# Kernel tuning notes

Measured on AMD Instinct MI355X. Metric: run time of the kernel, lower is better.

## Reference

```python
import jax, jax.numpy as jnp
import numpy as np

EPS_NORM = 1e-12  # torch F.normalize clamp_min eps
EPS_LOG = 1e-10


def setup_inputs() -> dict:
    key = jax.random.key(0)
    k1, k2 = jax.random.split(key)
    N, D = 12288, 128
    embeddings = jax.random.uniform(k1, (N, D), dtype=jnp.float32)
    adj = jax.random.uniform(k2, (N, N), dtype=jnp.float32)
    lambda_reg = jnp.float32(1.0)
    return {"embeddings": embeddings, "adj": adj, "lambda_reg": lambda_reg}


def reference(embeddings, adj, lambda_reg):
    # F.normalize(embeddings, dim=1, p=4): x / max(||x||_4, eps)
    norm4 = jnp.power(jnp.sum(jnp.abs(embeddings) ** 4, axis=1, keepdims=True), 0.25)
    e = embeddings / jnp.maximum(norm4, EPS_NORM)          # [N, D]
    log_p = jnp.log(e + EPS_LOG)                           # [N, D]
    p_log_p = jnp.sum(e * log_p, axis=1)                   # [N]
    cross = e @ log_p.T                                    # [N, N]
    kl = p_log_p[:, None] - cross                          # [N, N]
    # F.normalize(adj, p=1, dim=1): row-wise L1 normalization
    adj_n = adj / jnp.maximum(jnp.sum(jnp.abs(adj), axis=1, keepdims=True), EPS_NORM)
    return lambda_reg * jnp.sum(kl * adj_n)
```

## Files before the change

### kernel.cpp

```cpp
#include <hip/hip_runtime.h>
#include <hip/hip_bf16.h>

#define EPSN 1e-12f
#define EPSL 1e-10f
#define KSPLIT 64
#define KS 64

typedef __attribute__((ext_vector_type(8))) short short8;
typedef __attribute__((ext_vector_type(4))) float f32x4;

__device__ __forceinline__ unsigned short f2bf_rne(float f) {
  union { float f; unsigned u; } x; x.f = f;
  unsigned r = x.u + 0x7FFFu + ((x.u >> 16) & 1u);
  return (unsigned short)(r >> 16);
}

__global__ __launch_bounds__(256)
void prep_kernel(const float* __restrict__ emb, float* __restrict__ e,
                 unsigned short* __restrict__ lpB, float* __restrict__ plp,
                 float* __restrict__ S, float* __restrict__ v, int N) {
  int w = threadIdx.x >> 6, l = threadIdx.x & 63;
  int row = blockIdx.x * 4 + w;
  if (row >= N) return;
  const float* x = emb + (size_t)row * 128;
  float2 xv = *(const float2*)(x + 2 * l);
  float s4 = xv.x*xv.x*xv.x*xv.x + xv.y*xv.y*xv.y*xv.y;
  #pragma unroll
  for (int m = 1; m < 64; m <<= 1) s4 += __shfl_xor(s4, m);
  float denom = fmaxf(sqrtf(sqrtf(s4)), EPSN);
  float e0 = xv.x / denom, e1 = xv.y / denom;
  float lp0 = logf(e0 + EPSL), lp1 = logf(e1 + EPSL);
  e[(size_t)row * 128 + 2*l]     = e0;
  e[(size_t)row * 128 + 2*l + 1] = e1;
  int ksr = row >> 5, lhir = (row >> 3) & 3, jr = row & 7;
  int d0 = 2 * l, d1 = 2 * l + 1;
  lpB[((size_t)(ksr*8 + (d0>>4))*64 + (d0&15) + 16*lhir)*8 + jr] = f2bf_rne(lp0);
  lpB[((size_t)(ksr*8 + (d1>>4))*64 + (d1&15) + 16*lhir)*8 + jr] = f2bf_rne(lp1);
  float pl = e0 * lp0 + e1 * lp1;
  #pragma unroll
  for (int m = 1; m < 64; m <<= 1) pl += __shfl_xor(pl, m);
  if (l == 0) { plp[row] = pl; S[row] = 0.f; v[row] = 0.f; }
}

__global__ __launch_bounds__(256, 2)
void gemm_kernel(const float* __restrict__ adj, const float* __restrict__ e,
                 const unsigned short* __restrict__ lpB,
                 float* __restrict__ S, float* __restrict__ v, int N) {
  __shared__ unsigned short bsh[KS * 3 * 128];
  int w = threadIdx.x >> 6, l = threadIdx.x & 63;
  int l16 = l & 15, lhi = l >> 4;
  int wrow0 = blockIdx.x * 128 + w * 32;
  int kr = N / KSPLIT;
  int k0 = blockIdx.y * kr;
  int nsteps = kr / KS;

  {
    const short8* gB = (const short8*)(lpB + (size_t)k0 * 128);
    short8* sB = (short8*)bsh;
    #pragma unroll
    for (int i = 0; i < 12; ++i) {
      int idx = (w * 12 + i) * 64 + l;
      sB[idx] = gB[idx];
    }
  }

  f32x4 acc[2][8];
  #pragma unroll
  for (int i = 0; i < 2; ++i)
    #pragma unroll
    for (int j = 0; j < 8; ++j) acc[i][j] = (f32x4){0.f, 0.f, 0.f, 0.f};
  float sAcc[2] = {0.f, 0.f};

  const float* rp0 = adj + (size_t)(wrow0 + l16) * N + k0 + lhi * 8;
  const float* rp1 = rp0 + (size_t)16 * N;

  float4 ra[2][2][2], rb[2][2][2];

#define LOADA(buf, s)                                                   \
  {                                                                     \
    _Pragma("unroll")                                                   \
    for (int rt_ = 0; rt_ < 2; ++rt_) {                                 \
      const float* bp_ = (rt_ ? rp1 : rp0) + (s) * KS;                  \
      _Pragma("unroll")                                                 \
      for (int ks_ = 0; ks_ < 2; ++ks_) {                               \
        buf[rt_][ks_][0] = *(const float4*)(bp_ + ks_ * 32);            \
        buf[rt_][ks_][1] = *(const float4*)(bp_ + ks_ * 32 + 4);        \
      }                                                                 \
    }                                                                   \
  }

#define STEP(buf, s)                                                    \
  {                                                                     \
    _Pragma("unroll")                                                   \
    for (int ks_ = 0; ks_ < 2; ++ks_) {                                 \
      short8 bb_[8];                                                    \
      _Pragma("unroll")                                                 \
      for (int ct_ = 0; ct_ < 8; ++ct_)                                 \
        bb_[ct_] = *((const short8*)bsh + ((size_t)(((s)*2 + ks_)*8 + ct_))*64 + l); \
      short8 af_[2];                                                    \
      _Pragma("unroll")                                                 \
      for (int rt_ = 0; rt_ < 2; ++rt_) {                               \
        float4 x0_ = buf[rt_][ks_][0], x1_ = buf[rt_][ks_][1];          \
        sAcc[rt_] += ((x0_.x + x0_.y) + (x0_.z + x0_.w)) +              \
                     ((x1_.x + x1_.y) + (x1_.z + x1_.w));               \
        short8 t_;                                                      \
        t_[0] = (short)f2bf_rne(x0_.x); t_[1] = (short)f2bf_rne(x0_.y); \
        t_[2] = (short)f2bf_rne(x0_.z); t_[3] = (short)f2bf_rne(x0_.w); \
        t_[4] = (short)f2bf_rne(x1_.x); t_[5] = (short)f2bf_rne(x1_.y); \
        t_[6] = (short)f2bf_rne(x1_.z); t_[7] = (short)f2bf_rne(x1_.w); \
        af_[rt_] = t_;                                                  \
      }                                                                 \
      _Pragma("unroll")                                                 \
      for (int ct_ = 0; ct_ < 8; ++ct_) {                               \
        acc[0][ct_] = __builtin_amdgcn_mfma_f32_16x16x32_bf16(af_[0], bb_[ct_], acc[0][ct_], 0, 0, 0); \
        acc[1][ct_] = __builtin_amdgcn_mfma_f32_16x16x32_bf16(af_[1], bb_[ct_], acc[1][ct_], 0, 0, 0); \
      }                                                                 \
    }                                                                   \
  }

  LOADA(ra, 0);
  __syncthreads();

  for (int s = 0; s < nsteps; s += 2) {
    if (s + 1 < nsteps) LOADA(rb, s + 1);
    STEP(ra, s);
    if (s + 2 < nsteps) LOADA(ra, s + 2);
    if (s + 1 < nsteps) STEP(rb, s + 1);
  }

  #pragma unroll
  for (int rt = 0; rt < 2; ++rt) {
    float s = sAcc[rt];
    s += __shfl_xor(s, 16);
    s += __shfl_xor(s, 32);
    if (l < 16) atomicAdd(&S[wrow0 + rt * 16 + l], s);
  }

  #pragma unroll
  for (int rt = 0; rt < 2; ++rt) {
    #pragma unroll
    for (int r = 0; r < 4; ++r) {
      int row = wrow0 + rt * 16 + lhi * 4 + r;
      float p = 0.f;
      #pragma unroll
      for (int ct = 0; ct < 8; ++ct)
        p += e[(size_t)row * 128 + ct * 16 + l16] * acc[rt][ct][r];
      p += __shfl_xor(p, 1);
      p += __shfl_xor(p, 2);
      p += __shfl_xor(p, 4);
      p += __shfl_xor(p, 8);
      if (l16 == 0) atomicAdd(&v[row], p);
    }
  }
}

__global__ __launch_bounds__(1024)
void final_kernel(const float* __restrict__ plp, const float* __restrict__ S,
                  const float* __restrict__ v, const float* __restrict__ lam,
                  float* __restrict__ out, int N) {
  __shared__ float red[16];
  float acc = 0.f;
  for (int i = threadIdx.x; i < N; i += 1024) {
    float s = S[i], d = fmaxf(s, EPSN);
    acc += plp[i] * (s / d) - v[i] / d;
  }
  #pragma unroll
  for (int m = 1; m < 64; m <<= 1) acc += __shfl_xor(acc, m);
  int w = threadIdx.x >> 6, l = threadIdx.x & 63;
  if (l == 0) red[w] = acc;
  __syncthreads();
  if (threadIdx.x == 0) {
    float t = 0.f;
    #pragma unroll
    for (int i = 0; i < 16; ++i) t += red[i];
    out[0] = lam[0] * t;
  }
}

extern "C" void kernel_launch(void* const* d_in, const int* in_sizes, int n_in,
                              void* d_out, int out_size, void* d_ws, size_t ws_size,
                              hipStream_t stream) {
  const float* emb = (const float*)d_in[0];
  const float* adj = (const float*)d_in[1];
  const float* lam = (const float*)d_in[2];
  int N = in_sizes[0] / 128;

  char* ws = (char*)d_ws;
  float* e            = (float*)ws;
  unsigned short* lpB = (unsigned short*)(ws + (size_t)N * 512);
  float* plp          = (float*)(ws + (size_t)N * 768);
  float* S            = plp + N;
  float* v            = S + N;

  prep_kernel<<<(N + 3) / 4, 256, 0, stream>>>(emb, e, lpB, plp, S, v, N);
  dim3 grid(N / 128, KSPLIT);
  gemm_kernel<<<grid, 256, 0, stream>>>(adj, e, lpB, S, v, N);
  final_kernel<<<1, 1024, 0, stream>>>(plp, S, v, lam, (float*)d_out, N);
}
```

Measured before the change: 205.6 us.

## Stream B tiles through double-buffered LDS and reduce K-split count

```diff
diff --git a/kernel.cpp b/kernel.cpp
--- a/kernel.cpp
+++ b/kernel.cpp
@@ -3,7 +3,7 @@
 
 #define EPSN 1e-12f
 #define EPSL 1e-10f
-#define KSPLIT 64
+#define KSPLIT 16
 #define KS 64
 
 typedef __attribute__((ext_vector_type(8))) short short8;
@@ -42,27 +42,17 @@
   if (l == 0) { plp[row] = pl; S[row] = 0.f; v[row] = 0.f; }
 }
 
-__global__ __launch_bounds__(256, 2)
+__global__ __launch_bounds__(256, 3)
 void gemm_kernel(const float* __restrict__ adj, const float* __restrict__ e,
                  const unsigned short* __restrict__ lpB,
                  float* __restrict__ S, float* __restrict__ v, int N) {
-  __shared__ unsigned short bsh[KS * 3 * 128];
+  __shared__ unsigned short bsh[2][KS * 128];
   int w = threadIdx.x >> 6, l = threadIdx.x & 63;
   int l16 = l & 15, lhi = l >> 4;
   int wrow0 = blockIdx.x * 128 + w * 32;
   int kr = N / KSPLIT;
   int k0 = blockIdx.y * kr;
-  int nsteps = kr / KS;
-
-  {
-    const short8* gB = (const short8*)(lpB + (size_t)k0 * 128);
-    short8* sB = (short8*)bsh;
-    #pragma unroll
-    for (int i = 0; i < 12; ++i) {
-      int idx = (w * 12 + i) * 64 + l;
-      sB[idx] = gB[idx];
-    }
-  }
+  int nt = kr / KS;
 
   f32x4 acc[2][8];
   #pragma unroll
@@ -74,13 +64,14 @@
   const float* rp0 = adj + (size_t)(wrow0 + l16) * N + k0 + lhi * 8;
   const float* rp1 = rp0 + (size_t)16 * N;
 
-  float4 ra[2][2][2], rb[2][2][2];
-
-#define LOADA(buf, s)                                                   \
+  float4 aset0[2][2][2], aset1[2][2][2];
+  float4 rBs[2][4];
+
+#define LOADA(buf, t)                                                   \
   {                                                                     \
     _Pragma("unroll")                                                   \
     for (int rt_ = 0; rt_ < 2; ++rt_) {                                 \
-      const float* bp_ = (rt_ ? rp1 : rp0) + (s) * KS;                  \
+      const float* bp_ = (rt_ ? rp1 : rp0) + (t) * KS;                  \
       _Pragma("unroll")                                                 \
       for (int ks_ = 0; ks_ < 2; ++ks_) {                               \
         buf[rt_][ks_][0] = *(const float4*)(bp_ + ks_ * 32);            \
@@ -89,18 +80,35 @@
     }                                                                   \
   }
 
-#define STEP(buf, s)                                                    \
+#define LOADB(dst, t)                                                   \
+  {                                                                     \
+    const char* p_ = (const char*)lpB + (((size_t)(k0 + (t) * KS)) << 8) \
+                     + w * 4096 + l * 16;                               \
+    _Pragma("unroll")                                                   \
+    for (int i_ = 0; i_ < 4; ++i_)                                      \
+      dst[i_] = *(const float4*)(p_ + i_ * 1024);                       \
+  }
+
+#define WRITEB(bi, src)                                                 \
+  {                                                                     \
+    char* q_ = (char*)bsh[bi] + w * 4096 + l * 16;                      \
+    _Pragma("unroll")                                                   \
+    for (int i_ = 0; i_ < 4; ++i_)                                      \
+      *(float4*)(q_ + i_ * 1024) = src[i_];                             \
+  }
+
+#define STEP(abuf, bi)                                                  \
   {                                                                     \
     _Pragma("unroll")                                                   \
     for (int ks_ = 0; ks_ < 2; ++ks_) {                                 \
       short8 bb_[8];                                                    \
       _Pragma("unroll")                                                 \
       for (int ct_ = 0; ct_ < 8; ++ct_)                                 \
-        bb_[ct_] = *((const short8*)bsh + ((size_t)(((s)*2 + ks_)*8 + ct_))*64 + l); \
+        bb_[ct_] = *(const short8*)((char*)bsh[bi] + (ks_*8 + ct_)*1024 + l*16); \
       short8 af_[2];                                                    \
       _Pragma("unroll")                                                 \
       for (int rt_ = 0; rt_ < 2; ++rt_) {                               \
-        float4 x0_ = buf[rt_][ks_][0], x1_ = buf[rt_][ks_][1];          \
+        float4 x0_ = abuf[rt_][ks_][0], x1_ = abuf[rt_][ks_][1];        \
         sAcc[rt_] += ((x0_.x + x0_.y) + (x0_.z + x0_.w)) +              \
                      ((x1_.x + x1_.y) + (x1_.z + x1_.w));               \
         short8 t_;                                                      \
@@ -110,22 +118,41 @@
         t_[6] = (short)f2bf_rne(x1_.z); t_[7] = (short)f2bf_rne(x1_.w); \
         af_[rt_] = t_;                                                  \
       }                                                                 \
+      __builtin_amdgcn_s_setprio(1);                                    \
       _Pragma("unroll")                                                 \
       for (int ct_ = 0; ct_ < 8; ++ct_) {                               \
         acc[0][ct_] = __builtin_amdgcn_mfma_f32_16x16x32_bf16(af_[0], bb_[ct_], acc[0][ct_], 0, 0, 0); \
         acc[1][ct_] = __builtin_amdgcn_mfma_f32_16x16x32_bf16(af_[1], bb_[ct_], acc[1][ct_], 0, 0, 0); \
       }                                                                 \
+      __builtin_amdgcn_s_setprio(0);                                    \
     }                                                                   \
   }
 
-  LOADA(ra, 0);
-  __syncthreads();
-
-  for (int s = 0; s < nsteps; s += 2) {
-    if (s + 1 < nsteps) LOADA(rb, s + 1);
-    STEP(ra, s);
-    if (s + 2 < nsteps) LOADA(ra, s + 2);
-    if (s + 1 < nsteps) STEP(rb, s + 1);
+#define FENCE_BARRIER()                                                 \
+  {                                                                     \
+    asm volatile("s_waitcnt lgkmcnt(0)" ::: "memory");                  \
+    __builtin_amdgcn_s_barrier();                                       \
+    asm volatile("" ::: "memory");                                      \
+  }
+
+#define ITER(t, aset, bi)                                               \
+  {                                                                     \
+    STEP(aset, bi);                                                     \
+    if ((t) + 1 < nt) WRITEB((bi) ^ 1, rBs[((t) + 1) & 1]);             \
+    if ((t) + 2 < nt) { LOADB(rBs[(t) & 1], (t) + 2); LOADA(aset, (t) + 2); } \
+    FENCE_BARRIER();                                                    \
+  }
+
+  LOADB(rBs[0], 0);
+  LOADA(aset0, 0);
+  LOADB(rBs[1], 1);
+  LOADA(aset1, 1);
+  WRITEB(0, rBs[0]);
+  FENCE_BARRIER();
+
+  for (int t = 0; t < nt; t += 2) {
+    ITER(t, aset0, 0);
+    ITER(t + 1, aset1, 1);
   }
 
   #pragma unroll
```

New measurement: 516.1 us. 151% more time.

## Restructure GEMM to 32-row tiles with LDS-staged bf16 adj and streamed B

Applied to the files above, without the earlier changes.

```diff
diff --git a/kernel.cpp b/kernel.cpp
--- a/kernel.cpp
+++ b/kernel.cpp
@@ -3,8 +3,9 @@
 
 #define EPSN 1e-12f
 #define EPSL 1e-10f
-#define KSPLIT 64
-#define KS 64
+#define TILEM 32
+#define KSPLIT 2
+#define KS 256
 
 typedef __attribute__((ext_vector_type(8))) short short8;
 typedef __attribute__((ext_vector_type(4))) float f32x4;
@@ -16,7 +17,7 @@
 }
 
 __global__ __launch_bounds__(256)
-void prep_kernel(const float* __restrict__ emb, float* __restrict__ e,
+void prep_kernel(const float* __restrict__ emb, float* __restrict__ eC,
                  unsigned short* __restrict__ lpB, float* __restrict__ plp,
                  float* __restrict__ S, float* __restrict__ v, int N) {
   int w = threadIdx.x >> 6, l = threadIdx.x & 63;
@@ -30,10 +31,11 @@
   float denom = fmaxf(sqrtf(sqrtf(s4)), EPSN);
   float e0 = xv.x / denom, e1 = xv.y / denom;
   float lp0 = logf(e0 + EPSL), lp1 = logf(e1 + EPSL);
-  e[(size_t)row * 128 + 2*l]     = e0;
-  e[(size_t)row * 128 + 2*l + 1] = e1;
+  int Rg = row >> 4, lhig = (row >> 2) & 3, rg = row & 3;
+  int d0 = 2 * l, d1 = 2 * l + 1;
+  eC[(((size_t)Rg * 8 + (d0 >> 4)) * 64 + (d0 & 15) + 16 * lhig) * 4 + rg] = e0;
+  eC[(((size_t)Rg * 8 + (d1 >> 4)) * 64 + (d1 & 15) + 16 * lhig) * 4 + rg] = e1;
   int ksr = row >> 5, lhir = (row >> 3) & 3, jr = row & 7;
-  int d0 = 2 * l, d1 = 2 * l + 1;
   lpB[((size_t)(ksr*8 + (d0>>4))*64 + (d0&15) + 16*lhir)*8 + jr] = f2bf_rne(lp0);
   lpB[((size_t)(ksr*8 + (d1>>4))*64 + (d1&15) + 16*lhir)*8 + jr] = f2bf_rne(lp1);
   float pl = e0 * lp0 + e1 * lp1;
@@ -42,114 +44,115 @@
   if (l == 0) { plp[row] = pl; S[row] = 0.f; v[row] = 0.f; }
 }
 
-__global__ __launch_bounds__(256, 2)
-void gemm_kernel(const float* __restrict__ adj, const float* __restrict__ e,
+__global__ __launch_bounds__(256, 3)
+void gemm_kernel(const float* __restrict__ adj, const float* __restrict__ eC,
                  const unsigned short* __restrict__ lpB,
                  float* __restrict__ S, float* __restrict__ v, int N) {
-  __shared__ unsigned short bsh[KS * 3 * 128];
+  __shared__ unsigned short ash[2][TILEM * KS];
   int w = threadIdx.x >> 6, l = threadIdx.x & 63;
   int l16 = l & 15, lhi = l >> 4;
-  int wrow0 = blockIdx.x * 128 + w * 32;
+  int row0 = blockIdx.x * TILEM;
   int kr = N / KSPLIT;
   int k0 = blockIdx.y * kr;
-  int nsteps = kr / KS;
-
-  {
-    const short8* gB = (const short8*)(lpB + (size_t)k0 * 128);
-    short8* sB = (short8*)bsh;
-    #pragma unroll
-    for (int i = 0; i < 12; ++i) {
-      int idx = (w * 12 + i) * 64 + l;
-      sB[idx] = gB[idx];
-    }
-  }
-
-  f32x4 acc[2][8];
+  int nt = kr / KS;
+
+  f32x4 acc[2][2];
   #pragma unroll
   for (int i = 0; i < 2; ++i)
     #pragma unroll
-    for (int j = 0; j < 8; ++j) acc[i][j] = (f32x4){0.f, 0.f, 0.f, 0.f};
-  float sAcc[2] = {0.f, 0.f};
-
-  const float* rp0 = adj + (size_t)(wrow0 + l16) * N + k0 + lhi * 8;
-  const float* rp1 = rp0 + (size_t)16 * N;
-
-  float4 ra[2][2][2], rb[2][2][2];
-
-#define LOADA(buf, s)                                                   \
+    for (int j = 0; j < 2; ++j) acc[i][j] = (f32x4){0.f, 0.f, 0.f, 0.f};
+  float sAcc[8];
+  #pragma unroll
+  for (int j = 0; j < 8; ++j) sAcc[j] = 0.f;
+
+  const float* aBase = adj + (size_t)(row0 + 8 * w) * N + k0 + 4 * l;
+  float4 ar[8];
+
+#define LOADA(t)                                                        \
   {                                                                     \
     _Pragma("unroll")                                                   \
-    for (int rt_ = 0; rt_ < 2; ++rt_) {                                 \
-      const float* bp_ = (rt_ ? rp1 : rp0) + (s) * KS;                  \
-      _Pragma("unroll")                                                 \
-      for (int ks_ = 0; ks_ < 2; ++ks_) {                               \
-        buf[rt_][ks_][0] = *(const float4*)(bp_ + ks_ * 32);            \
-        buf[rt_][ks_][1] = *(const float4*)(bp_ + ks_ * 32 + 4);        \
-      }                                                                 \
+    for (int j_ = 0; j_ < 8; ++j_)                                      \
+      ar[j_] = *(const float4*)(aBase + (size_t)j_ * N + (size_t)(t) * KS); \
+  }
+
+#define STAGE(bi)                                                       \
+  {                                                                     \
+    char* base_ = (char*)ash[bi];                                       \
+    _Pragma("unroll")                                                   \
+    for (int j_ = 0; j_ < 8; ++j_) {                                    \
+      float4 x_ = ar[j_];                                               \
+      sAcc[j_] += (x_.x + x_.y) + (x_.z + x_.w);                        \
+      unsigned p0_ = (unsigned)f2bf_rne(x_.x) | ((unsigned)f2bf_rne(x_.y) << 16); \
+      unsigned p1_ = (unsigned)f2bf_rne(x_.z) | ((unsigned)f2bf_rne(x_.w) << 16); \
+      int rl_ = 8 * w + j_;                                             \
+      int off_ = rl_ * 512 + ((l * 8) ^ ((rl_ & 7) << 4));              \
+      *(uint2*)(base_ + off_) = make_uint2(p0_, p1_);                   \
     }                                                                   \
   }
 
-#define STEP(buf, s)                                                    \
+#define MSTEP(bi, t)                                                    \
   {                                                                     \
+    const char* base_ = (const char*)ash[bi];                           \
+    size_t fb_ = (size_t)((k0 + (t) * KS) >> 5) * 8;                    \
     _Pragma("unroll")                                                   \
-    for (int ks_ = 0; ks_ < 2; ++ks_) {                                 \
-      short8 bb_[8];                                                    \
-      _Pragma("unroll")                                                 \
-      for (int ct_ = 0; ct_ < 8; ++ct_)                                 \
-        bb_[ct_] = *((const short8*)bsh + ((size_t)(((s)*2 + ks_)*8 + ct_))*64 + l); \
-      short8 af_[2];                                                    \
-      _Pragma("unroll")                                                 \
-      for (int rt_ = 0; rt_ < 2; ++rt_) {                               \
-        float4 x0_ = buf[rt_][ks_][0], x1_ = buf[rt_][ks_][1];          \
-        sAcc[rt_] += ((x0_.x + x0_.y) + (x0_.z + x0_.w)) +              \
-                     ((x1_.x + x1_.y) + (x1_.z + x1_.w));               \
-        short8 t_;                                                      \
-        t_[0] = (short)f2bf_rne(x0_.x); t_[1] = (short)f2bf_rne(x0_.y); \
-        t_[2] = (short)f2bf_rne(x0_.z); t_[3] = (short)f2bf_rne(x0_.w); \
-        t_[4] = (short)f2bf_rne(x1_.x); t_[5] = (short)f2bf_rne(x1_.y); \
-        t_[6] = (short)f2bf_rne(x1_.z); t_[7] = (short)f2bf_rne(x1_.w); \
-        af_[rt_] = t_;                                                  \
-      }                                                                 \
-      _Pragma("unroll")                                                 \
-      for (int ct_ = 0; ct_ < 8; ++ct_) {                               \
-        acc[0][ct_] = __builtin_amdgcn_mfma_f32_16x16x32_bf16(af_[0], bb_[ct_], acc[0][ct_], 0, 0, 0); \
-        acc[1][ct_] = __builtin_amdgcn_mfma_f32_16x16x32_bf16(af_[1], bb_[ct_], acc[1][ct_], 0, 0, 0); \
-      }                                                                 \
+    for (int kg_ = 0; kg_ < 8; ++kg_) {                                 \
+      int ao_ = (kg_ * 64 + lhi * 16) ^ ((l16 & 7) << 4);               \
+      short8 a0_ = *(const short8*)(base_ + l16 * 512 + ao_);           \
+      short8 a1_ = *(const short8*)(base_ + (16 + l16) * 512 + ao_);    \
+      short8 b0_ = ((const short8*)lpB)[(fb_ + (size_t)kg_ * 8 + 2 * w) * 64 + l];     \
+      short8 b1_ = ((const short8*)lpB)[(fb_ + (size_t)kg_ * 8 + 2 * w + 1) * 64 + l]; \
+      acc[0][0] = __builtin_amdgcn_mfma_f32_16x16x32_bf16(a0_, b0_, acc[0][0], 0, 0, 0); \
+      acc[0][1] = __builtin_amdgcn_mfma_f32_16x16x32_bf16(a0_, b1_, acc[0][1], 0, 0, 0); \
+      acc[1][0] = __builtin_amdgcn_mfma_f32_16x16x32_bf16(a1_, b0_, acc[1][0], 0, 0, 0); \
+      acc[1][1] = __builtin_amdgcn_mfma_f32_16x16x32_bf16(a1_, b1_, acc[1][1], 0, 0, 0); \
     }                                                                   \
   }
 
-  LOADA(ra, 0);
+  LOADA(0);
+  STAGE(0);
   __syncthreads();
 
-  for (int s = 0; s < nsteps; s += 2) {
-    if (s + 1 < nsteps) LOADA(rb, s + 1);
-    STEP(ra, s);
-    if (s + 2 < nsteps) LOADA(ra, s + 2);
-    if (s + 1 < nsteps) STEP(rb, s + 1);
+  for (int t = 0; t < nt; ++t) {
+    if (t + 1 < nt) LOADA(t + 1);
+    MSTEP(t & 1, t);
+    if (t + 1 < nt) STAGE((t + 1) & 1);
+    __syncthreads();
+  }
+
+  #pragma unroll
+  for (int j = 0; j < 8; ++j) {
+    float s = sAcc[j];
+    #pragma unroll
+    for (int m = 1; m < 64; m <<= 1) s += __shfl_xor(s, m);
+    if (l == 0) atomicAdd(&S[row0 + 8 * w + j], s);
   }
 
   #pragma unroll
   for (int rt = 0; rt < 2; ++rt) {
-    float s = sAcc[rt];
-    s += __shfl_xor(s, 16);
-    s += __shfl_xor(s, 32);
-    if (l < 16) atomicAdd(&S[wrow0 + rt * 16 + l], s);
-  }
-
-  #pragma unroll
-  for (int rt = 0; rt < 2; ++rt) {
-    #pragma unroll
-    for (int r = 0; r < 4; ++r) {
-      int row = wrow0 + rt * 16 + lhi * 4 + r;
-      float p = 0.f;
-      #pragma unroll
-      for (int ct = 0; ct < 8; ++ct)
-        p += e[(size_t)row * 128 + ct * 16 + l16] * acc[rt][ct][r];
-      p += __shfl_xor(p, 1);
-      p += __shfl_xor(p, 2);
-      p += __shfl_xor(p, 4);
-      p += __shfl_xor(p, 8);
-      if (l16 == 0) atomicAdd(&v[row], p);
+    int R = (row0 >> 4) + rt;
+    float p0 = 0.f, p1 = 0.f, p2 = 0.f, p3 = 0.f;
+    #pragma unroll
+    for (int c = 0; c < 2; ++c) {
+      int ctg = 2 * w + c;
+      float4 ef = *(const float4*)(eC + (((size_t)R * 8 + ctg) * 64 + l) * 4);
+      p0 += ef.x * acc[rt][c][0];
+      p1 += ef.y * acc[rt][c][1];
+      p2 += ef.z * acc[rt][c][2];
+      p3 += ef.w * acc[rt][c][3];
+    }
+    #pragma unroll
+    for (int m = 1; m < 16; m <<= 1) {
+      p0 += __shfl_xor(p0, m);
+      p1 += __shfl_xor(p1, m);
+      p2 += __shfl_xor(p2, m);
+      p3 += __shfl_xor(p3, m);
+    }
+    if (l16 == 0) {
+      int rb = row0 + rt * 16 + lhi * 4;
+      atomicAdd(&v[rb + 0], p0);
+      atomicAdd(&v[rb + 1], p1);
+      atomicAdd(&v[rb + 2], p2);
+      atomicAdd(&v[rb + 3], p3);
     }
   }
 }
@@ -186,14 +189,14 @@
   int N = in_sizes[0] / 128;
 
   char* ws = (char*)d_ws;
-  float* e            = (float*)ws;
+  float* eC           = (float*)ws;
   unsigned short* lpB = (unsigned short*)(ws + (size_t)N * 512);
   float* plp          = (float*)(ws + (size_t)N * 768);
   float* S            = plp + N;
   float* v            = S + N;
 
-  prep_kernel<<<(N + 3) / 4, 256, 0, stream>>>(emb, e, lpB, plp, S, v, N);
-  dim3 grid(N / 128, KSPLIT);
-  gemm_kernel<<<grid, 256, 0, stream>>>(adj, e, lpB, S, v, N);
+  prep_kernel<<<(N + 3) / 4, 256, 0, stream>>>(emb, eC, lpB, plp, S, v, N);
+  dim3 grid(N / TILEM, KSPLIT);
+  gemm_kernel<<<grid, 256, 0, stream>>>(adj, eC, lpB, S, v, N);
   final_kernel<<<1, 1024, 0, stream>>>(plp, S, v, lam, (float*)d_out, N);
 }
```

Measured after the change: 221.3 us. +7.7%, slower.
